# Kernel optimization log

Measured on AMD Instinct MI355X. Metric: run time of the kernel, lower is better.

## Reference

```python
import jax, jax.numpy as jnp
import numpy as np
from jax import lax

B, H, W = 8, 64, 64
C = 192          # in_channel == out_channel
CI = 384         # inner_channel = int(2.0 * C)


def setup_inputs() -> dict:
    key = jax.random.key(0)
    ks = jax.random.split(key, 8)
    s = 0.02
    return {
        "x": jax.random.normal(ks[0], (B, H, W, C), jnp.float32),
        "Win": jax.random.normal(ks[1], (C, 2 * CI), jnp.float32) * s,
        "conv_w": jax.random.normal(ks[2], (CI, 1, 3, 3), jnp.float32) * s,
        "conv_b": jnp.zeros((CI,), jnp.float32),
        "Wout": jax.random.normal(ks[3], (CI, C), jnp.float32) * s,
        "Wm1": jax.random.normal(ks[4], (C, 4 * C), jnp.float32) * s,
        "bm1": jnp.zeros((4 * C,), jnp.float32),
        "Wm2": jax.random.normal(ks[5], (4 * C, C), jnp.float32) * s,
        "bm2": jnp.zeros((C,), jnp.float32),
    }


def reference(x, Win, conv_w, conv_b, Wout, Wm1, bm1, Wm2, bm2):
    silu = jax.nn.silu
    shortcut = x                                   # [B,H,W,C], norm1 is Identity (norm=None)
    xz = jnp.einsum('bhwc,cd->bhwd', x, Win)       # in_proj (no bias) -> [B,H,W,2*CI]
    x1, z = jnp.split(xz, 2, axis=-1)
    # channel_recover -> [B,CI,H,W], depthwise conv + silu
    xc = jnp.transpose(x1, (0, 3, 1, 2))
    xc = lax.conv_general_dilated(xc, conv_w, (1, 1), 'SAME',
                                  feature_group_count=CI,
                                  dimension_numbers=('NCHW', 'OIHW', 'NCHW'))
    xc = silu(xc + conv_b[None, :, None, None])
    L = H * W
    # cross_scan: K=2 views (row-major and transposed), doubled by flip_scan -> [B,4,CI,L]
    x0 = xc.reshape(B, CI, L)
    xt = jnp.transpose(xc, (0, 1, 3, 2)).reshape(B, CI, L)
    x_cross = jnp.stack([x0, xt], axis=1)
    xs = jnp.concatenate([x_cross, jnp.flip(x_cross, axis=-1)], axis=1)
    out_y = xs  # ssm() is abstract in MBaseBlock -> identity passthrough
    # scan_proj (CrossMerge): undo flips and permutations, sum branches
    inv_y = jnp.flip(out_y[:, 2:4], axis=-1)

    def unperm(v):  # branch scanned in transposed (W,H) order -> back to (H,W)
        return jnp.transpose(v.reshape(B, CI, W, H), (0, 1, 3, 2)).reshape(B, CI, L)

    y = out_y[:, 0] + inv_y[:, 0] + unperm(out_y[:, 1]) + unperm(inv_y[:, 1])
    y = jnp.transpose(y, (0, 2, 1)).reshape(B, H, W, CI)  # norm2 is Identity
    y = y * silu(z)                                       # gate
    out = jnp.einsum('bhwc,cd->bhwd', y, Wout)            # out_proj (no bias)
    out = shortcut + out                                  # dropout/drop_path are Identity
    # dense is Identity (in_channel == out_channel); MLP branch 192->768->192
    h = silu(jnp.einsum('bhwc,cd->bhwd', out, Wm1) + bm1)
    mlp = jnp.einsum('bhwd,dc->bhwc', h, Wm2) + bm2
    return out + mlp
```

## Files before the change

kernel.cpp:

```cpp
#include <hip/hip_runtime.h>
#include <hip/hip_bf16.h>

#define BDIM 8
#define HDIM 64
#define WDIM 64
#define CDIM 192
#define CIDIM 384
#define MTOK (BDIM * HDIM * WDIM)

using bf16 = __hip_bfloat16;
typedef __attribute__((ext_vector_type(8))) short short8;
typedef __attribute__((ext_vector_type(4))) float f32x4;

__device__ __forceinline__ float silu_f(float v) { return v / (1.0f + __expf(-v)); }
__device__ __forceinline__ float bf2f(short s) {
    union { unsigned u; float f; } x; x.u = ((unsigned)(unsigned short)s) << 16; return x.f;
}

__device__ __forceinline__ void gload_lds16(const bf16* g, bf16* l) {
    __builtin_amdgcn_global_load_lds(
        (const __attribute__((address_space(1))) void*)g,
        (__attribute__((address_space(3))) void*)l, 16, 0, 0);
}

#define NSTRIPE 40
template <int EPI>
__launch_bounds__(256, 2)
__global__ void gemm_k192_p(const bf16* __restrict__ A, const bf16* __restrict__ BT,
                            const float* __restrict__ bias,
                            bf16* __restrict__ outB, bf16* __restrict__ outB2)
{
    __shared__ bf16 As[2][64 * 192];
    __shared__ bf16 Bs[64 * 192];

    const int bid = blockIdx.x;
    const int n   = bid / NSTRIPE;
    const int s   = bid % NSTRIPE;
    const int n0  = n * 64;

    const int tid  = threadIdx.x;
    const int lane = tid & 63;
    const int wv   = tid >> 6;
    const int wm   = wv >> 1;
    const int wn   = wv & 1;

    int soff[6];
    #pragma unroll
    for (int i = 0; i < 6; ++i) {
        const int ci   = wv * 6 + i;
        const int c    = ci * 64 + lane;
        const int row  = c / 24;
        const int slot = c - row * 24;
        const int lsl  = slot ^ (row & 7);
        soff[i] = row * 192 + lsl * 8;
    }

    #pragma unroll
    for (int i = 0; i < 6; ++i)
        gload_lds16(BT + (size_t)n0 * 192 + soff[i], &Bs[(wv * 6 + i) * 512]);

    #pragma unroll
    for (int i = 0; i < 6; ++i)
        gload_lds16(A + (size_t)(s * 64) * 192 + soff[i], &As[0][(wv * 6 + i) * 512]);
    __syncthreads();

    const int mloc[2] = { wm * 32 + (lane & 15), wm * 32 + 16 + (lane & 15) };
    const int nloc[2] = { wn * 32 + (lane & 15), wn * 32 + 16 + (lane & 15) };
    const bool isZ = (EPI == 0) && (n0 >= CIDIM);
    bf16* dst        = (EPI == 0) ? (isZ ? outB2 : outB) : outB;
    const int stride = (EPI == 0) ? CIDIM : 768;
    const int col0   = (EPI == 0) ? (isZ ? n0 - CIDIM : n0) : n0;

    int cur = 0;
    for (int mt = s; mt < 512; mt += NSTRIPE) {
        const int nmt = mt + NSTRIPE;
        if (nmt < 512) {
            const bf16* a1 = A + (size_t)(nmt * 64) * 192;
            bf16* db = As[cur ^ 1];
            #pragma unroll
            for (int i = 0; i < 6; ++i)
                gload_lds16(a1 + soff[i], &db[(wv * 6 + i) * 512]);
        }

        const bf16* la = As[cur];
        f32x4 acc[2][2] = {};
        #pragma unroll
        for (int ks = 0; ks < 6; ++ks) {
            const int t = ks * 4 + (lane >> 4);
            short8 af[2], bfr[2];
            #pragma unroll
            for (int mi = 0; mi < 2; ++mi) {
                const int m = mloc[mi];
                af[mi] = *reinterpret_cast<const short8*>(&la[m * 192 + ((t ^ (m & 7)) << 3)]);
            }
            #pragma unroll
            for (int ni = 0; ni < 2; ++ni) {
                const int nn = nloc[ni];
                bfr[ni] = *reinterpret_cast<const short8*>(&Bs[nn * 192 + ((t ^ (nn & 7)) << 3)]);
            }
            #pragma unroll
            for (int mi = 0; mi < 2; ++mi)
                #pragma unroll
                for (int ni = 0; ni < 2; ++ni)
                    acc[mi][ni] = __builtin_amdgcn_mfma_f32_16x16x32_bf16(
                        af[mi], bfr[ni], acc[mi][ni], 0, 0, 0);
        }

        const int m0   = mt * 64;
        const int rowb = m0 + wm * 32 + (lane >> 4) * 4;
        const int colb = col0 + wn * 32 + (lane & 15);
        #pragma unroll
        for (int mi = 0; mi < 2; ++mi) {
            #pragma unroll
            for (int ni = 0; ni < 2; ++ni) {
                const int c = colb + ni * 16;
                #pragma unroll
                for (int j = 0; j < 4; ++j) {
                    const int row = rowb + mi * 16 + j;
                    float v = acc[mi][ni][j];
                    if constexpr (EPI == 0) {
                        if (isZ) v = 4.0f * silu_f(v);
                    } else {
                        v = silu_f(v + bias[n0 + (c - col0)]);
                    }
                    dst[(size_t)row * stride + c] = __float2bfloat16(v);
                }
            }
        }

        __syncthreads();
        cur ^= 1;
    }
}

template <int EPI>
__launch_bounds__(256, 4)
__global__ void gemm_mfma(const bf16* __restrict__ A, const bf16* __restrict__ BT,
                          const float* __restrict__ bias,
                          const float* __restrict__ residF,
                          const bf16* __restrict__ residB,
                          float* __restrict__ outF, bf16* __restrict__ outB,
                          int M, int N, int K, int NX)
{
    __shared__ bf16 As[128 * 64];
    __shared__ bf16 Bs[64 * 64];

    const int bid = blockIdx.x;
    const int c8  = bid & 7;
    const int kq  = bid >> 3;
    const int bx  = kq % NX;
    const int by  = (kq / NX) * 8 + c8;
    const int m0  = by * 128;
    const int n0  = bx * 64;

    const int tid  = threadIdx.x;
    const int lane = tid & 63;
    const int wv   = tid >> 6;
    const int wm   = wv >> 1;
    const int wn   = wv & 1;

    const int srow  = lane >> 3;
    const int sslot = lane & 7;

    f32x4 acc[4][2] = {};

    for (int k0 = 0; k0 < K; k0 += 64) {
        #pragma unroll
        for (int i = 0; i < 4; ++i) {
            const int rb = wv * 32 + i * 8;
            const int r  = rb + srow;
            gload_lds16(A + (size_t)(m0 + r) * K + k0 + ((sslot ^ (r & 7)) << 3),
                        &As[rb * 64]);
        }
        #pragma unroll
        for (int i = 0; i < 2; ++i) {
            const int rb = wv * 16 + i * 8;
            const int r  = rb + srow;
            gload_lds16(BT + (size_t)(n0 + r) * K + k0 + ((sslot ^ (r & 7)) << 3),
                        &Bs[rb * 64]);
        }
        __syncthreads();

        #pragma unroll
        for (int kk = 0; kk < 2; ++kk) {
            const int t = kk * 4 + (lane >> 4);
            short8 af[4], bfr[2];
            #pragma unroll
            for (int mi = 0; mi < 4; ++mi) {
                const int m = wm * 64 + mi * 16 + (lane & 15);
                af[mi] = *reinterpret_cast<const short8*>(&As[m * 64 + ((t ^ (m & 7)) << 3)]);
            }
            #pragma unroll
            for (int ni = 0; ni < 2; ++ni) {
                const int n = wn * 32 + ni * 16 + (lane & 15);
                bfr[ni] = *reinterpret_cast<const short8*>(&Bs[n * 64 + ((t ^ (n & 7)) << 3)]);
            }
            #pragma unroll
            for (int mi = 0; mi < 4; ++mi)
                #pragma unroll
                for (int ni = 0; ni < 2; ++ni)
                    acc[mi][ni] = __builtin_amdgcn_mfma_f32_16x16x32_bf16(
                        af[mi], bfr[ni], acc[mi][ni], 0, 0, 0);
        }
        __syncthreads();
    }

    const int colb = n0 + wn * 32 + (lane & 15);
    const int rowb = m0 + wm * 64 + (lane >> 4) * 4;
    #pragma unroll
    for (int mi = 0; mi < 4; ++mi) {
        #pragma unroll
        for (int ni = 0; ni < 2; ++ni) {
            const int c = colb + ni * 16;
            #pragma unroll
            for (int j = 0; j < 4; ++j) {
                const int row = rowb + mi * 16 + j;
                const size_t off = (size_t)row * N + c;
                const float v = acc[mi][ni][j];
                if constexpr (EPI == 1) {
                    outB[off] = __float2bfloat16(v + residF[off]);
                } else {
                    outF[off] = v + bias[c] + bf2f(*(const short*)&residB[off]);
                }
            }
        }
    }
}

__launch_bounds__(256)
__global__ void dwconv_gate_v6(const bf16* __restrict__ x1, const bf16* __restrict__ sz,
                               const float* __restrict__ wT, const float* __restrict__ conv_b,
                               bf16* __restrict__ y)
{
    const int bid = blockIdx.x;
    const int swz = (bid & 7) * ((int)gridDim.x >> 3) + (bid >> 3);
    const int f   = swz * 256 + threadIdx.x;
    const int m   = f / 48;
    const int cg  = f - m * 48;
    const int c0  = cg * 8;
    const int h   = (m >> 6) & 63;
    const int w   = m & 63;

    float acc[8];
    {
        const f32x4 ba = *reinterpret_cast<const f32x4*>(&conv_b[c0]);
        const f32x4 bb = *reinterpret_cast<const f32x4*>(&conv_b[c0 + 4]);
        acc[0] = ba[0]; acc[1] = ba[1]; acc[2] = ba[2]; acc[3] = ba[3];
        acc[4] = bb[0]; acc[5] = bb[1]; acc[6] = bb[2]; acc[7] = bb[3];
    }

    #pragma unroll
    for (int r = 0; r < 3; ++r) {
        const int hh = h + r - 1;
        if (hh < 0 || hh >= HDIM) continue;
        #pragma unroll
        for (int dw = 0; dw < 3; ++dw) {
            const int ww = w + dw - 1;
            if (ww < 0 || ww >= WDIM) continue;
            const int mm  = m + (r - 1) * WDIM + (dw - 1);
            const int tap = r * 3 + dw;
            const short8 t = *reinterpret_cast<const short8*>(&x1[(size_t)mm * CIDIM + c0]);
            const f32x4 wa = *reinterpret_cast<const f32x4*>(&wT[tap * CIDIM + c0]);
            const f32x4 wb = *reinterpret_cast<const f32x4*>(&wT[tap * CIDIM + c0 + 4]);
            acc[0] += bf2f(t[0]) * wa[0]; acc[1] += bf2f(t[1]) * wa[1];
            acc[2] += bf2f(t[2]) * wa[2]; acc[3] += bf2f(t[3]) * wa[3];
            acc[4] += bf2f(t[4]) * wb[0]; acc[5] += bf2f(t[5]) * wb[1];
            acc[6] += bf2f(t[6]) * wb[2]; acc[7] += bf2f(t[7]) * wb[3];
        }
    }

    const short8 g = *reinterpret_cast<const short8*>(&sz[(size_t)m * CIDIM + c0]);
    bf16 tmp[8];
    #pragma unroll
    for (int j = 0; j < 8; ++j)
        tmp[j] = __float2bfloat16(silu_f(acc[j]) * bf2f(g[j]));
    *reinterpret_cast<short8*>(&y[(size_t)m * CIDIM + c0]) =
        *reinterpret_cast<const short8*>(tmp);
}

#define SZ_WIN  (192 * 768)
#define SZ_WOUT (384 * 192)
#define SZ_WM1  (192 * 768)
#define SZ_WM2  (768 * 192)
#define SZ_CW   (CIDIM * 9)
#define XCVT    (MTOK * CDIM / 4)
#define SZ_ALL  (XCVT + SZ_WIN + SZ_WOUT + SZ_WM1 + SZ_WM2 + SZ_CW)

__launch_bounds__(256)
__global__ void prep_all(const float* __restrict__ x, const float* __restrict__ Win,
                         const float* __restrict__ Wout, const float* __restrict__ Wm1,
                         const float* __restrict__ Wm2, const float* __restrict__ convw,
                         bf16* __restrict__ xb, bf16* __restrict__ WinT,
                         bf16* __restrict__ WoutT, bf16* __restrict__ Wm1T,
                         bf16* __restrict__ Wm2T, float* __restrict__ wTc)
{
    int idx = blockIdx.x * 256 + threadIdx.x;
    if (idx < XCVT) {
        const int i = idx * 4;
        const float4 v = *reinterpret_cast<const float4*>(&x[i]);
        xb[i + 0] = __float2bfloat16(v.x);
        xb[i + 1] = __float2bfloat16(v.y);
        xb[i + 2] = __float2bfloat16(v.z);
        xb[i + 3] = __float2bfloat16(v.w);
        return;
    }
    idx -= XCVT;
    if (idx < SZ_WIN) {
        const int r = idx / 768, c = idx % 768;
        WinT[(size_t)c * 192 + r] = __float2bfloat16(Win[idx]);
        return;
    }
    idx -= SZ_WIN;
    if (idx < SZ_WOUT) {
        const int r = idx / 192, c = idx % 192;
        WoutT[(size_t)c * 384 + r] = __float2bfloat16(Wout[idx]);
        return;
    }
    idx -= SZ_WOUT;
    if (idx < SZ_WM1) {
        const int r = idx / 768, c = idx % 768;
        Wm1T[(size_t)c * 192 + r] = __float2bfloat16(Wm1[idx]);
        return;
    }
    idx -= SZ_WM1;
    if (idx < SZ_WM2) {
        const int r = idx / 192, c = idx % 192;
        Wm2T[(size_t)c * 768 + r] = __float2bfloat16(Wm2[idx]);
        return;
    }
    idx -= SZ_WM2;
    if (idx < SZ_CW) {
        const int ci = idx / 9, t = idx % 9;
        wTc[t * CIDIM + ci] = convw[idx];
    }
}

extern "C" void kernel_launch(void* const* d_in, const int* in_sizes, int n_in,
                              void* d_out, int out_size, void* d_ws, size_t ws_size,
                              hipStream_t stream)
{
    const float* x      = (const float*)d_in[0];
    const float* Win    = (const float*)d_in[1];
    const float* conv_w = (const float*)d_in[2];
    const float* conv_b = (const float*)d_in[3];
    const float* Wout   = (const float*)d_in[4];
    const float* Wm1    = (const float*)d_in[5];
    const float* bm1    = (const float*)d_in[6];
    const float* Wm2    = (const float*)d_in[7];
    const float* bm2    = (const float*)d_in[8];
    float* out = (float*)d_out;

    char* ws = (char*)d_ws;
    size_t o = 0;
    bf16*  xb    = (bf16*)(ws + o); o += (size_t)MTOK * CDIM * 2;
    bf16*  WinT  = (bf16*)(ws + o); o += (size_t)768 * 192 * 2;
    bf16*  WoutT = (bf16*)(ws + o); o += (size_t)192 * 384 * 2;
    bf16*  Wm1T  = (bf16*)(ws + o); o += (size_t)768 * 192 * 2;
    bf16*  Wm2T  = (bf16*)(ws + o); o += (size_t)192 * 768 * 2;
    float* wTc   = (float*)(ws + o); o += (size_t)9 * CIDIM * 4;
    bf16*  ws_x1 = (bf16*)(ws + o); o += (size_t)MTOK * CIDIM * 2;
    bf16*  ws_sz = (bf16*)(ws + o); o += (size_t)MTOK * CIDIM * 2;
    bf16*  ws_y  = (bf16*)(ws + o); o += (size_t)MTOK * CIDIM * 2;
    bf16*  ws_ob = (bf16*)(ws + o); o += (size_t)MTOK * CDIM * 2;
    bf16*  ws_h  = ws_x1;

    prep_all<<<dim3((SZ_ALL + 255) / 256), dim3(256), 0, stream>>>(
        x, Win, Wout, Wm1, Wm2, conv_w, xb, WinT, WoutT, Wm1T, Wm2T, wTc);

    gemm_k192_p<0><<<dim3(12 * NSTRIPE), dim3(256), 0, stream>>>(
        xb, WinT, nullptr, ws_x1, ws_sz);

    dwconv_gate_v6<<<dim3(MTOK * 48 / 256), dim3(256), 0, stream>>>(
        ws_x1, ws_sz, wTc, conv_b, ws_y);

    gemm_mfma<1><<<dim3(3 * 256), dim3(256), 0, stream>>>(
        ws_y, WoutT, nullptr, x, nullptr, nullptr, ws_ob, MTOK, CDIM, CIDIM, 3);

    gemm_k192_p<2><<<dim3(12 * NSTRIPE), dim3(256), 0, stream>>>(
        ws_ob, Wm1T, bm1, ws_h, nullptr);

    gemm_mfma<3><<<dim3(3 * 256), dim3(256), 0, stream>>>(
        ws_h, Wm2T, bm2, nullptr, ws_ob, out, nullptr, MTOK, CDIM, 768, 3);
}
```

Measured before the change: 121.8 us.

## Fuse MLP up- and down-projection into one kernel keeping hidden tile in LDS

Replaces the separate Wm1 GEMM (writing the 768-wide hidden activation to global memory) and the Wm2 GEMM with a single kernel. Each block computes a 64-row tile of the hidden activation into LDS, then multiplies it by Wm2 and adds the bias and residual. This removes the global write and read of the hidden tensor and one launch. In exchange it uses about 120KB of LDS per block (one block per CU), reads weight B-fragments directly from global memory without LDS staging, and launches only 512 blocks.

```diff
diff --git a/kernel.cpp b/kernel.cpp
--- a/kernel.cpp
+++ b/kernel.cpp
@@ -22,6 +22,8 @@
         (const __attribute__((address_space(1))) void*)g,
         (__attribute__((address_space(3))) void*)l, 16, 0, 0);
 }
+
+#define MFMA16(a, b, c) __builtin_amdgcn_mfma_f32_16x16x32_bf16(a, b, c, 0, 0, 0)
 
 #define NSTRIPE 40
 template <int EPI>
@@ -58,7 +60,6 @@
     #pragma unroll
     for (int i = 0; i < 6; ++i)
         gload_lds16(BT + (size_t)n0 * 192 + soff[i], &Bs[(wv * 6 + i) * 512]);
-
     #pragma unroll
     for (int i = 0; i < 6; ++i)
         gload_lds16(A + (size_t)(s * 64) * 192 + soff[i], &As[0][(wv * 6 + i) * 512]);
@@ -102,8 +103,7 @@
             for (int mi = 0; mi < 2; ++mi)
                 #pragma unroll
                 for (int ni = 0; ni < 2; ++ni)
-                    acc[mi][ni] = __builtin_amdgcn_mfma_f32_16x16x32_bf16(
-                        af[mi], bfr[ni], acc[mi][ni], 0, 0, 0);
+                    acc[mi][ni] = MFMA16(af[mi], bfr[ni], acc[mi][ni]);
         }
 
         const int m0   = mt * 64;
@@ -136,10 +136,7 @@
 template <int EPI>
 __launch_bounds__(256, 4)
 __global__ void gemm_mfma(const bf16* __restrict__ A, const bf16* __restrict__ BT,
-                          const float* __restrict__ bias,
-                          const float* __restrict__ residF,
-                          const bf16* __restrict__ residB,
-                          float* __restrict__ outF, bf16* __restrict__ outB,
+                          const float* __restrict__ residF, bf16* __restrict__ outB,
                           int M, int N, int K, int NX)
 {
     __shared__ bf16 As[128 * 64];
@@ -199,8 +196,7 @@
             for (int mi = 0; mi < 4; ++mi)
                 #pragma unroll
                 for (int ni = 0; ni < 2; ++ni)
-                    acc[mi][ni] = __builtin_amdgcn_mfma_f32_16x16x32_bf16(
-                        af[mi], bfr[ni], acc[mi][ni], 0, 0, 0);
+                    acc[mi][ni] = MFMA16(af[mi], bfr[ni], acc[mi][ni]);
         }
         __syncthreads();
     }
@@ -216,12 +212,111 @@
             for (int j = 0; j < 4; ++j) {
                 const int row = rowb + mi * 16 + j;
                 const size_t off = (size_t)row * N + c;
-                const float v = acc[mi][ni][j];
-                if constexpr (EPI == 1) {
-                    outB[off] = __float2bfloat16(v + residF[off]);
-                } else {
-                    outF[off] = v + bias[c] + bf2f(*(const short*)&residB[off]);
+                outB[off] = __float2bfloat16(acc[mi][ni][j] + residF[off]);
+            }
+        }
+    }
+}
+
+__launch_bounds__(256, 1)
+__global__ void fused_mlp(const bf16* __restrict__ ob, const bf16* __restrict__ Wm1T,
+                          const bf16* __restrict__ Wm2T, const float* __restrict__ bm1,
+                          const float* __restrict__ bm2, float* __restrict__ out)
+{
+    __shared__ bf16 obs[64 * 192];
+    __shared__ bf16 hs[64 * 768];
+
+    const int m0   = blockIdx.x * 64;
+    const int tid  = threadIdx.x;
+    const int lane = tid & 63;
+    const int wv   = tid >> 6;
+    const int l15  = lane & 15;
+    const int l4   = lane >> 4;
+
+    #pragma unroll
+    for (int i = 0; i < 6; ++i) {
+        const int ci   = wv * 6 + i;
+        const int c    = ci * 64 + lane;
+        const int row  = c / 24;
+        const int slot = c - row * 24;
+        gload_lds16(ob + (size_t)(m0 + row) * 192 + (slot ^ (row & 7)) * 8,
+                    &obs[ci * 512]);
+    }
+    __syncthreads();
+
+    #pragma unroll
+    for (int cc = 0; cc < 3; ++cc) {
+        const int nc = wv * 3 + cc;
+        f32x4 hacc[4][4] = {};
+        #pragma unroll
+        for (int ks = 0; ks < 6; ++ks) {
+            short8 af[4];
+            #pragma unroll
+            for (int mi = 0; mi < 4; ++mi) {
+                const int r = mi * 16 + l15;
+                af[mi] = *reinterpret_cast<const short8*>(
+                    &obs[r * 192 + (((ks * 4 + l4) ^ (r & 7)) << 3)]);
+            }
+            #pragma unroll
+            for (int ni = 0; ni < 4; ++ni) {
+                const short8 b = *reinterpret_cast<const short8*>(
+                    Wm1T + (size_t)(nc * 64 + ni * 16 + l15) * 192 + (ks * 4 + l4) * 8);
+                #pragma unroll
+                for (int mi = 0; mi < 4; ++mi)
+                    hacc[mi][ni] = MFMA16(af[mi], b, hacc[mi][ni]);
+            }
+        }
+        #pragma unroll
+        for (int ni = 0; ni < 4; ++ni) {
+            const int col = nc * 64 + ni * 16 + l15;
+            const float bb = bm1[col];
+            #pragma unroll
+            for (int mi = 0; mi < 4; ++mi) {
+                #pragma unroll
+                for (int j = 0; j < 4; ++j) {
+                    const int r  = mi * 16 + l4 * 4 + j;
+                    const int ch = (col >> 3) ^ (r & 7);
+                    hs[r * 768 + ch * 8 + (col & 7)] =
+                        __float2bfloat16(silu_f(hacc[mi][ni][j] + bb));
                 }
+            }
+        }
+    }
+    __syncthreads();
+
+    const int c0w = wv * 48;
+    f32x4 facc[4][3] = {};
+    for (int ks = 0; ks < 24; ++ks) {
+        short8 ha[4];
+        #pragma unroll
+        for (int mi = 0; mi < 4; ++mi) {
+            const int r  = mi * 16 + l15;
+            const int ch = (ks * 4 + l4) ^ (r & 7);
+            ha[mi] = *reinterpret_cast<const short8*>(&hs[r * 768 + ch * 8]);
+        }
+        #pragma unroll
+        for (int ni = 0; ni < 3; ++ni) {
+            const short8 b = *reinterpret_cast<const short8*>(
+                Wm2T + (size_t)(c0w + ni * 16 + l15) * 768 + ks * 32 + l4 * 8);
+            #pragma unroll
+            for (int mi = 0; mi < 4; ++mi)
+                facc[mi][ni] = MFMA16(ha[mi], b, facc[mi][ni]);
+        }
+    }
+
+    #pragma unroll
+    for (int ni = 0; ni < 3; ++ni) {
+        const int col = c0w + ni * 16 + l15;
+        const float b2 = bm2[col];
+        #pragma unroll
+        for (int mi = 0; mi < 4; ++mi) {
+            #pragma unroll
+            for (int j = 0; j < 4; ++j) {
+                const int r  = mi * 16 + l4 * 4 + j;
+                const int ch = (col >> 3) ^ (r & 7);
+                const float resid = bf2f(*reinterpret_cast<const short*>(
+                    &obs[r * 192 + ch * 8 + (col & 7)]));
+                out[(size_t)(m0 + r) * 192 + col] = facc[mi][ni][j] + b2 + resid;
             }
         }
     }
@@ -362,7 +457,6 @@
     bf16*  ws_sz = (bf16*)(ws + o); o += (size_t)MTOK * CIDIM * 2;
     bf16*  ws_y  = (bf16*)(ws + o); o += (size_t)MTOK * CIDIM * 2;
     bf16*  ws_ob = (bf16*)(ws + o); o += (size_t)MTOK * CDIM * 2;
-    bf16*  ws_h  = ws_x1;
 
     prep_all<<<dim3((SZ_ALL + 255) / 256), dim3(256), 0, stream>>>(
         x, Win, Wout, Wm1, Wm2, conv_w, xb, WinT, WoutT, Wm1T, Wm2T, wTc);
@@ -374,11 +468,8 @@
         ws_x1, ws_sz, wTc, conv_b, ws_y);
 
     gemm_mfma<1><<<dim3(3 * 256), dim3(256), 0, stream>>>(
-        ws_y, WoutT, nullptr, x, nullptr, nullptr, ws_ob, MTOK, CDIM, CIDIM, 3);
-
-    gemm_k192_p<2><<<dim3(12 * NSTRIPE), dim3(256), 0, stream>>>(
-        ws_ob, Wm1T, bm1, ws_h, nullptr);
-
-    gemm_mfma<3><<<dim3(3 * 256), dim3(256), 0, stream>>>(
-        ws_h, Wm2T, bm2, nullptr, ws_ob, out, nullptr, MTOK, CDIM, 768, 3);
-}
+        ws_y, WoutT, x, ws_ob, MTOK, CDIM, CIDIM, 3);
+
+    fused_mlp<<<dim3(MTOK / 64), dim3(256), 0, stream>>>(
+        ws_ob, Wm1T, Wm2T, bm1, bm2, out);
+}
```

Result: slower. 137.0 us (+12.5%).
